# Performance work log

Hardware: AMD Instinct MI355X
Metric: run time of the kernel (lower is better)

Reference implementation:

```python
import jax, jax.numpy as jnp
import numpy as np

N, E = 50000, 800000
D_IN, H, D_OUT = 64, 64, 32
NEG_SLOPE = 0.2


def setup_inputs() -> dict:
    key = jax.random.key(0)
    ks = jax.random.split(key, 20)
    inp = {
        "x": jax.random.normal(ks[0], (N, D_IN), dtype=jnp.float32),
        "edge_index": jax.random.randint(ks[1], (2, E), 0, N, dtype=jnp.int32),
    }
    def lin(k, fan_in, fan_out):
        s = 1.0 / np.sqrt(fan_in)
        return jax.random.uniform(k, (fan_in, fan_out), jnp.float32, -s, s)
    # GAT layer params: W [in,H], att_src [H], att_dst [H], bias [H]
    dims_in = [D_IN, H, H]
    for i in range(3):
        inp[f"W{i+1}"] = lin(ks[2 + 4 * i], dims_in[i], H)
        inp[f"a_src{i+1}"] = jax.random.normal(ks[3 + 4 * i], (H,), jnp.float32) * 0.1
        inp[f"a_dst{i+1}"] = jax.random.normal(ks[4 + 4 * i], (H,), jnp.float32) * 0.1
        inp[f"b{i+1}"] = jnp.zeros((H,), jnp.float32)
    inp["lin1_W"] = lin(ks[14], H, H)
    inp["lin1_b"] = jnp.zeros((H,), jnp.float32)
    inp["lin2_W"] = lin(ks[15], H, D_OUT)
    inp["lin2_b"] = jnp.zeros((D_OUT,), jnp.float32)
    return inp


def gat_layer(x, src, dst, W, a_src, a_dst, b):
    h = x @ W                                   # [N, H]
    alpha_s = (h * a_src).sum(-1)               # [N]
    alpha_d = (h * a_dst).sum(-1)               # [N]
    e = jax.nn.leaky_relu(alpha_s[src] + alpha_d[dst], NEG_SLOPE)  # [E]
    m = jax.lax.stop_gradient(jax.ops.segment_max(e, dst, num_segments=N))
    w = jnp.exp(e - m[dst])                     # [E]
    denom = jax.ops.segment_sum(w, dst, num_segments=N)
    alpha = w / denom[dst]                      # segment softmax over incoming edges
    out = jax.ops.segment_sum(alpha[:, None] * h[src], dst, num_segments=N)
    return out + b


def reference(x, edge_index, W1, a_src1, a_dst1, b1, W2, a_src2, a_dst2, b2,
              W3, a_src3, a_dst3, b3, lin1_W, lin1_b, lin2_W, lin2_b):
    src, dst = edge_index[0], edge_index[1]
    h = jax.nn.relu(gat_layer(x, src, dst, W1, a_src1, a_dst1, b1))
    h = jax.nn.relu(gat_layer(h, src, dst, W2, a_src2, a_dst2, b2))
    h = jax.nn.relu(gat_layer(h, src, dst, W3, a_src3, a_dst3, b3))
    h = jax.nn.relu(h @ lin1_W + lin1_b)
    return h @ lin2_W + lin2_b
```

## Files before the change

kernel.cpp:

```cpp
#include <hip/hip_runtime.h>

#define NEG_SLOPE 0.2f
#define NBUCK 256

template <bool RELU, bool WANT_ALPHA>
__global__ __launch_bounds__(256) void gemm64(
    const float* __restrict__ x, const float* __restrict__ W,
    const float* __restrict__ bias,
    const float* __restrict__ a_src, const float* __restrict__ a_dst,
    float* __restrict__ out, float* __restrict__ alpha_s,
    float* __restrict__ alpha_d, int N)
{
    __shared__ float Xs[64][68];
    __shared__ float Ws[64][64];

    const int row0 = blockIdx.x * 64;

    for (int i = threadIdx.x; i < 1024; i += 256)
        ((float4*)Ws)[i] = ((const float4*)W)[i];
    for (int i = threadIdx.x; i < 1024; i += 256) {
        int r = i >> 4, c4 = (i & 15) * 4;
        float4 v = {0.f, 0.f, 0.f, 0.f};
        if (row0 + r < N) v = *(const float4*)&x[(size_t)(row0 + r) * 64 + c4];
        *(float4*)&Xs[r][c4] = v;
    }
    __syncthreads();

    const int tx = threadIdx.x & 15;
    const int ty = threadIdx.x >> 4;

    float acc[4][4] = {{0.f,0.f,0.f,0.f},{0.f,0.f,0.f,0.f},
                       {0.f,0.f,0.f,0.f},{0.f,0.f,0.f,0.f}};

#pragma unroll 8
    for (int k = 0; k < 64; ++k) {
        const float4 wv = *(const float4*)&Ws[k][tx * 4];
        const float x0 = Xs[ty * 4 + 0][k];
        const float x1 = Xs[ty * 4 + 1][k];
        const float x2 = Xs[ty * 4 + 2][k];
        const float x3 = Xs[ty * 4 + 3][k];
        acc[0][0] += x0 * wv.x; acc[0][1] += x0 * wv.y;
        acc[0][2] += x0 * wv.z; acc[0][3] += x0 * wv.w;
        acc[1][0] += x1 * wv.x; acc[1][1] += x1 * wv.y;
        acc[1][2] += x1 * wv.z; acc[1][3] += x1 * wv.w;
        acc[2][0] += x2 * wv.x; acc[2][1] += x2 * wv.y;
        acc[2][2] += x2 * wv.z; acc[2][3] += x2 * wv.w;
        acc[3][0] += x3 * wv.x; acc[3][1] += x3 * wv.y;
        acc[3][2] += x3 * wv.z; acc[3][3] += x3 * wv.w;
    }

    float4 bv = {0.f, 0.f, 0.f, 0.f};
    if (bias) bv = *(const float4*)&bias[tx * 4];

#pragma unroll
    for (int i = 0; i < 4; ++i) {
        const int r = row0 + ty * 4 + i;
        if (r < N) {
            float4 o;
            o.x = acc[i][0] + bv.x; o.y = acc[i][1] + bv.y;
            o.z = acc[i][2] + bv.z; o.w = acc[i][3] + bv.w;
            if (RELU) {
                o.x = fmaxf(o.x, 0.f); o.y = fmaxf(o.y, 0.f);
                o.z = fmaxf(o.z, 0.f); o.w = fmaxf(o.w, 0.f);
            }
            *(float4*)&out[(size_t)r * 64 + tx * 4] = o;
        }
    }

    if (WANT_ALPHA) {
        const float4 asv = *(const float4*)&a_src[tx * 4];
        const float4 adv = *(const float4*)&a_dst[tx * 4];
#pragma unroll
        for (int i = 0; i < 4; ++i) {
            float s = acc[i][0]*asv.x + acc[i][1]*asv.y
                    + acc[i][2]*asv.z + acc[i][3]*asv.w;
            float d = acc[i][0]*adv.x + acc[i][1]*adv.y
                    + acc[i][2]*adv.z + acc[i][3]*adv.w;
#pragma unroll
            for (int off = 1; off < 16; off <<= 1) {
                s += __shfl_xor(s, off, 16);
                d += __shfl_xor(d, off, 16);
            }
            const int r = row0 + ty * 4 + i;
            if (tx == 0 && r < N) { alpha_s[r] = s; alpha_d[r] = d; }
        }
    }
}

__global__ __launch_bounds__(256) void gemm_head(
    const float* __restrict__ X, const float* __restrict__ W1,
    const float* __restrict__ b1, const float* __restrict__ W2,
    const float* __restrict__ b2, float* __restrict__ out, int N)
{
    __shared__ float Xs[64][68];
    __shared__ float W1s[64][64];
    __shared__ float W2s[64][32];

    const int row0 = blockIdx.x * 64;

    for (int i = threadIdx.x; i < 1024; i += 256)
        ((float4*)W1s)[i] = ((const float4*)W1)[i];
    for (int i = threadIdx.x; i < 512; i += 256)
        ((float4*)W2s)[i] = ((const float4*)W2)[i];
    for (int i = threadIdx.x; i < 1024; i += 256) {
        int r = i >> 4, c4 = (i & 15) * 4;
        float4 v = {0.f, 0.f, 0.f, 0.f};
        if (row0 + r < N) v = *(const float4*)&X[(size_t)(row0 + r) * 64 + c4];
        *(float4*)&Xs[r][c4] = v;
    }
    __syncthreads();

    const int tx = threadIdx.x & 15;
    const int ty = threadIdx.x >> 4;

    float acc[4][4] = {{0,0,0,0},{0,0,0,0},{0,0,0,0},{0,0,0,0}};
#pragma unroll 8
    for (int k = 0; k < 64; ++k) {
        const float4 wv = *(const float4*)&W1s[k][tx * 4];
        const float x0 = Xs[ty * 4 + 0][k];
        const float x1 = Xs[ty * 4 + 1][k];
        const float x2 = Xs[ty * 4 + 2][k];
        const float x3 = Xs[ty * 4 + 3][k];
        acc[0][0] += x0 * wv.x; acc[0][1] += x0 * wv.y;
        acc[0][2] += x0 * wv.z; acc[0][3] += x0 * wv.w;
        acc[1][0] += x1 * wv.x; acc[1][1] += x1 * wv.y;
        acc[1][2] += x1 * wv.z; acc[1][3] += x1 * wv.w;
        acc[2][0] += x2 * wv.x; acc[2][1] += x2 * wv.y;
        acc[2][2] += x2 * wv.z; acc[2][3] += x2 * wv.w;
        acc[3][0] += x3 * wv.x; acc[3][1] += x3 * wv.y;
        acc[3][2] += x3 * wv.z; acc[3][3] += x3 * wv.w;
    }

    const float4 bv = *(const float4*)&b1[tx * 4];
    __syncthreads();
#pragma unroll
    for (int i = 0; i < 4; ++i) {
        Xs[ty * 4 + i][tx * 4 + 0] = fmaxf(acc[i][0] + bv.x, 0.f);
        Xs[ty * 4 + i][tx * 4 + 1] = fmaxf(acc[i][1] + bv.y, 0.f);
        Xs[ty * 4 + i][tx * 4 + 2] = fmaxf(acc[i][2] + bv.z, 0.f);
        Xs[ty * 4 + i][tx * 4 + 3] = fmaxf(acc[i][3] + bv.w, 0.f);
    }
    __syncthreads();

    float a2[4][2] = {{0,0},{0,0},{0,0},{0,0}};
#pragma unroll 8
    for (int k = 0; k < 64; ++k) {
        const float2 wv = *(const float2*)&W2s[k][tx * 2];
        const float t0 = Xs[ty * 4 + 0][k];
        const float t1 = Xs[ty * 4 + 1][k];
        const float t2 = Xs[ty * 4 + 2][k];
        const float t3 = Xs[ty * 4 + 3][k];
        a2[0][0] += t0 * wv.x; a2[0][1] += t0 * wv.y;
        a2[1][0] += t1 * wv.x; a2[1][1] += t1 * wv.y;
        a2[2][0] += t2 * wv.x; a2[2][1] += t2 * wv.y;
        a2[3][0] += t3 * wv.x; a2[3][1] += t3 * wv.y;
    }
    const float2 b2v = *(const float2*)&b2[tx * 2];
#pragma unroll
    for (int i = 0; i < 4; ++i) {
        const int r = row0 + ty * 4 + i;
        if (r < N) {
            float2 o;
            o.x = a2[i][0] + b2v.x;
            o.y = a2[i][1] + b2v.y;
            *(float2*)&out[(size_t)r * 32 + tx * 2] = o;
        }
    }
}

__global__ __launch_bounds__(256) void bucket_hist(
    const int* __restrict__ ei, int E, int* __restrict__ bhist)
{
    __shared__ int h[NBUCK];
    const int t = threadIdx.x;
    h[t] = 0;
    __syncthreads();
    for (int e = blockIdx.x * 256 + t; e < E; e += gridDim.x * 256)
        atomicAdd(&h[((unsigned)ei[E + e]) >> 8], 1);
    __syncthreads();
    if (h[t]) atomicAdd(&bhist[t], h[t]);
}

#define PC_EPT 8
#define PC_TILE 2048
__global__ __launch_bounds__(256) void partition_coarse(
    const int* __restrict__ ei, int E, const int* __restrict__ bhist,
    int* __restrict__ gcurs, int* __restrict__ pairs)
{
    __shared__ int sc[NBUCK];
    __shared__ int hist[NBUCK];
    __shared__ int base[NBUCK];
    const int t = threadIdx.x;

    const int bh = bhist[t];
    sc[t] = bh; __syncthreads();
    for (int off = 1; off < 256; off <<= 1) {
        int v = sc[t];
        if (t >= off) v += sc[t - off];
        __syncthreads(); sc[t] = v; __syncthreads();
    }
    const int bbase = sc[t] - bh;
    hist[t] = 0;
    __syncthreads();

    const int tile0 = blockIdx.x * PC_TILE;
    int sv[PC_EPT], dv[PC_EPT], rk[PC_EPT];
#pragma unroll
    for (int i = 0; i < PC_EPT; ++i) {
        const int e = tile0 + i * 256 + t;
        if (e < E) {
            sv[i] = ei[e];
            dv[i] = ei[E + e];
            rk[i] = atomicAdd(&hist[dv[i] >> 8], 1);
        } else dv[i] = -1;
    }
    __syncthreads();
    if (hist[t] > 0) base[t] = bbase + atomicAdd(&gcurs[t], hist[t]);
    __syncthreads();
#pragma unroll
    for (int i = 0; i < PC_EPT; ++i) {
        if (dv[i] >= 0) {
            const int b = dv[i] >> 8;
            pairs[base[b] + rk[i]] = sv[i] | ((dv[i] & 255) << 16);
        }
    }
}

__global__ __launch_bounds__(256) void fine_scatter(
    const int* __restrict__ bhist, const int* __restrict__ pairs,
    int N, int E, int* __restrict__ row_off, int* __restrict__ csr_src)
{
    __shared__ int sc[NBUCK];
    __shared__ int cnt[NBUCK];
    __shared__ int cur[NBUCK];
    const int t = threadIdx.x, b = blockIdx.x;

    const int bh = bhist[t];
    sc[t] = bh; __syncthreads();
    for (int off = 1; off < 256; off <<= 1) {
        int v = sc[t];
        if (t >= off) v += sc[t - off];
        __syncthreads(); sc[t] = v; __syncthreads();
    }
    sc[t] -= bh;
    cnt[t] = 0;
    __syncthreads();

    const int sb = sc[b];
    const int se = sb + bhist[b];

    for (int p = sb + t; p < se; p += 256)
        atomicAdd(&cnt[pairs[p] >> 16], 1);
    __syncthreads();

    const int c = cnt[t];
    cur[t] = c; __syncthreads();
    for (int off = 1; off < 256; off <<= 1) {
        int v = cur[t];
        if (t >= off) v += cur[t - off];
        __syncthreads(); cur[t] = v; __syncthreads();
    }
    const int node_off = sb + cur[t] - c;
    __syncthreads();
    cur[t] = node_off;
    const int n = b * 256 + t;
    if (n < N) row_off[n] = node_off;
    if (b == gridDim.x - 1 && t == 0) row_off[N] = E;
    __syncthreads();

    for (int p = sb + t; p < se; p += 256) {
        const int v = pairs[p];
        const int pos = atomicAdd(&cur[v >> 16], 1);
        csr_src[pos] = v & 0xFFFF;
    }
}

__global__ __launch_bounds__(256) void gat_aggregate(
    const int* __restrict__ row_off, const int* __restrict__ csr_src,
    const float* __restrict__ h, const float* __restrict__ as,
    const float* __restrict__ ad, const float* __restrict__ bias,
    float* __restrict__ out, int N)
{
    const int wv = (blockIdx.x * 256 + threadIdx.x) >> 6;
    if (wv >= N) return;
    const int d    = wv;
    const int lane = threadIdx.x & 63;
    const int g    = lane >> 4;
    const int gl   = lane & 15;

    const int beg = row_off[d], end = row_off[d + 1];
    const float add = ad[d];

    float  den  = 0.f;
    float4 acc0 = {0.f, 0.f, 0.f, 0.f};
    float4 acc1 = {0.f, 0.f, 0.f, 0.f};

    int s0 = (beg     + g < end) ? csr_src[beg     + g] : 0;
    int s1 = (beg + 4 + g < end) ? csr_src[beg + 4 + g] : 0;

    for (int e0 = beg; e0 < end; e0 += 8) {
        const bool v0 = (e0     + g < end);
        const bool v1 = (e0 + 4 + g < end);
        const int  cs0 = s0, cs1 = s1;

        const int n0 = e0 +  8 + g;
        const int n1 = e0 + 12 + g;
        s0 = (n0 < end) ? csr_src[n0] : 0;
        s1 = (n1 < end) ? csr_src[n1] : 0;

        const float4 h0 = *(const float4*)&h[(size_t)cs0 * 64 + gl * 4];
        const float4 h1 = *(const float4*)&h[(size_t)cs1 * 64 + gl * 4];
        const float  a0 = as[cs0];
        const float  a1 = as[cs1];

        float ev0 = a0 + add;
        ev0 = (ev0 >= 0.f) ? ev0 : NEG_SLOPE * ev0;
        float ev1 = a1 + add;
        ev1 = (ev1 >= 0.f) ? ev1 : NEG_SLOPE * ev1;

        const float w0 = v0 ? __expf(ev0) : 0.f;
        const float w1 = v1 ? __expf(ev1) : 0.f;

        den += w0 + w1;
        acc0.x += w0 * h0.x; acc0.y += w0 * h0.y;
        acc0.z += w0 * h0.z; acc0.w += w0 * h0.w;
        acc1.x += w1 * h1.x; acc1.y += w1 * h1.y;
        acc1.z += w1 * h1.z; acc1.w += w1 * h1.w;
    }

    float4 acc;
    acc.x = acc0.x + acc1.x; acc.y = acc0.y + acc1.y;
    acc.z = acc0.z + acc1.z; acc.w = acc0.w + acc1.w;

#pragma unroll
    for (int off = 16; off <= 32; off <<= 1) {
        acc.x += __shfl_xor(acc.x, off, 64);
        acc.y += __shfl_xor(acc.y, off, 64);
        acc.z += __shfl_xor(acc.z, off, 64);
        acc.w += __shfl_xor(acc.w, off, 64);
        den   += __shfl_xor(den,   off, 64);
    }

    if (g == 0) {
        const float4 bvv = *(const float4*)&bias[gl * 4];
        const float inv = (den > 0.f) ? (1.f / den) : 0.f;
        float4 o;
        o.x = fmaxf(acc.x * inv + bvv.x, 0.f);
        o.y = fmaxf(acc.y * inv + bvv.y, 0.f);
        o.z = fmaxf(acc.z * inv + bvv.z, 0.f);
        o.w = fmaxf(acc.w * inv + bvv.w, 0.f);
        *(float4*)&out[(size_t)d * 64 + gl * 4] = o;
    }
}

extern "C" void kernel_launch(void* const* d_in, const int* in_sizes, int n_in,
                              void* d_out, int out_size, void* d_ws, size_t ws_size,
                              hipStream_t stream)
{
    const float* x  = (const float*)d_in[0];
    const int*   ei = (const int*)d_in[1];
    const float* W[3]    = {(const float*)d_in[2], (const float*)d_in[6],  (const float*)d_in[10]};
    const float* asrc[3] = {(const float*)d_in[3], (const float*)d_in[7],  (const float*)d_in[11]};
    const float* adst[3] = {(const float*)d_in[4], (const float*)d_in[8],  (const float*)d_in[12]};
    const float* bia[3]  = {(const float*)d_in[5], (const float*)d_in[9],  (const float*)d_in[13]};
    const float* lin1W = (const float*)d_in[14];
    const float* lin1b = (const float*)d_in[15];
    const float* lin2W = (const float*)d_in[16];
    const float* lin2b = (const float*)d_in[17];

    const int N = in_sizes[0] / 64;
    const int E = in_sizes[1] / 2;
    const int B = (N + 255) / 256;

    float* X       = (float*)d_ws;
    float* H       = X + (size_t)N * 64;
    float* AS      = H + (size_t)N * 64;
    float* AD      = AS + N;
    int*   row_off = (int*)(AD + N);
    int*   csr_src = row_off + (N + 1);
    int*   bhist   = csr_src + E;
    int*   gcurs   = bhist + 256;
    int*   pairs   = (int*)H;

    const int g64_grid = (N + 63) / 64;
    const int agg_grid = (N + 3) / 4;
    const int pc_grid  = (E + PC_TILE - 1) / PC_TILE;

    hipMemsetAsync(bhist, 0, 512 * sizeof(int), stream);
    bucket_hist<<<256, 256, 0, stream>>>(ei, E, bhist);
    partition_coarse<<<pc_grid, 256, 0, stream>>>(ei, E, bhist, gcurs, pairs);
    fine_scatter<<<B, 256, 0, stream>>>(bhist, pairs, N, E, row_off, csr_src);

    for (int l = 0; l < 3; ++l) {
        const float* in_act = (l == 0) ? x : X;
        gemm64<false, true><<<g64_grid, 256, 0, stream>>>(
            in_act, W[l], nullptr, asrc[l], adst[l], H, AS, AD, N);
        gat_aggregate<<<agg_grid, 256, 0, stream>>>(
            row_off, csr_src, H, AS, AD, bia[l], X, N);
    }

    gemm_head<<<g64_grid, 256, 0, stream>>>(
        X, lin1W, lin1b, lin2W, lin2b, (float*)d_out, N);
}
```

Measured before the change: 209.2 us.

## Fuse bucket histogram into first GEMM and unroll aggregation to 16 edges

Removes the standalone bucket_hist kernel and folds the destination-bucket histogram into the first layer's gemm64 launch, run by its first 256 blocks. The pairs buffer moves out of H into its own workspace region so the layer-1 GEMM output survives partitioning. The aggregation loop now processes four edge groups per iteration instead of two, giving more independent gathers in flight per wave. Costs include an extra shared histogram buffer, extra registers in the aggregator, and a larger workspace.

```diff
diff --git a/kernel.cpp b/kernel.cpp
--- a/kernel.cpp
+++ b/kernel.cpp
@@ -3,16 +3,17 @@
 #define NEG_SLOPE 0.2f
 #define NBUCK 256
 
-template <bool RELU, bool WANT_ALPHA>
+template <bool WANT_ALPHA, bool DO_HIST>
 __global__ __launch_bounds__(256) void gemm64(
     const float* __restrict__ x, const float* __restrict__ W,
-    const float* __restrict__ bias,
     const float* __restrict__ a_src, const float* __restrict__ a_dst,
     float* __restrict__ out, float* __restrict__ alpha_s,
-    float* __restrict__ alpha_d, int N)
+    float* __restrict__ alpha_d, int N,
+    const int* __restrict__ ei, int E, int* __restrict__ bhist)
 {
     __shared__ float Xs[64][68];
     __shared__ float Ws[64][64];
+    __shared__ int   hsh[NBUCK];
 
     const int row0 = blockIdx.x * 64;
 
@@ -24,6 +25,7 @@
         if (row0 + r < N) v = *(const float4*)&x[(size_t)(row0 + r) * 64 + c4];
         *(float4*)&Xs[r][c4] = v;
     }
+    if (DO_HIST && blockIdx.x < 256) hsh[threadIdx.x] = 0;
     __syncthreads();
 
     const int tx = threadIdx.x & 15;
@@ -49,20 +51,11 @@
         acc[3][2] += x3 * wv.z; acc[3][3] += x3 * wv.w;
     }
 
-    float4 bv = {0.f, 0.f, 0.f, 0.f};
-    if (bias) bv = *(const float4*)&bias[tx * 4];
-
 #pragma unroll
     for (int i = 0; i < 4; ++i) {
         const int r = row0 + ty * 4 + i;
         if (r < N) {
-            float4 o;
-            o.x = acc[i][0] + bv.x; o.y = acc[i][1] + bv.y;
-            o.z = acc[i][2] + bv.z; o.w = acc[i][3] + bv.w;
-            if (RELU) {
-                o.x = fmaxf(o.x, 0.f); o.y = fmaxf(o.y, 0.f);
-                o.z = fmaxf(o.z, 0.f); o.w = fmaxf(o.w, 0.f);
-            }
+            float4 o = {acc[i][0], acc[i][1], acc[i][2], acc[i][3]};
             *(float4*)&out[(size_t)r * 64 + tx * 4] = o;
         }
     }
@@ -84,6 +77,14 @@
             const int r = row0 + ty * 4 + i;
             if (tx == 0 && r < N) { alpha_s[r] = s; alpha_d[r] = d; }
         }
+    }
+
+    if (DO_HIST && blockIdx.x < 256) {
+        __syncthreads();
+        for (int e = blockIdx.x * 256 + threadIdx.x; e < E; e += 256 * 256)
+            atomicAdd(&hsh[((unsigned)ei[E + e]) >> 8], 1);
+        __syncthreads();
+        if (hsh[threadIdx.x]) atomicAdd(&bhist[threadIdx.x], hsh[threadIdx.x]);
     }
 }
 
@@ -168,19 +169,6 @@
     }
 }
 
-__global__ __launch_bounds__(256) void bucket_hist(
-    const int* __restrict__ ei, int E, int* __restrict__ bhist)
-{
-    __shared__ int h[NBUCK];
-    const int t = threadIdx.x;
-    h[t] = 0;
-    __syncthreads();
-    for (int e = blockIdx.x * 256 + t; e < E; e += gridDim.x * 256)
-        atomicAdd(&h[((unsigned)ei[E + e]) >> 8], 1);
-    __syncthreads();
-    if (h[t]) atomicAdd(&bhist[t], h[t]);
-}
-
 #define PC_EPT 8
 #define PC_TILE 2048
 __global__ __launch_bounds__(256) void partition_coarse(
@@ -292,45 +280,61 @@
     const float add = ad[d];
 
     float  den  = 0.f;
-    float4 acc0 = {0.f, 0.f, 0.f, 0.f};
-    float4 acc1 = {0.f, 0.f, 0.f, 0.f};
-
-    int s0 = (beg     + g < end) ? csr_src[beg     + g] : 0;
-    int s1 = (beg + 4 + g < end) ? csr_src[beg + 4 + g] : 0;
-
-    for (int e0 = beg; e0 < end; e0 += 8) {
-        const bool v0 = (e0     + g < end);
-        const bool v1 = (e0 + 4 + g < end);
-        const int  cs0 = s0, cs1 = s1;
-
-        const int n0 = e0 +  8 + g;
-        const int n1 = e0 + 12 + g;
-        s0 = (n0 < end) ? csr_src[n0] : 0;
-        s1 = (n1 < end) ? csr_src[n1] : 0;
+    float4 acc0 = {0.f,0.f,0.f,0.f}, acc1 = {0.f,0.f,0.f,0.f};
+    float4 acc2 = {0.f,0.f,0.f,0.f}, acc3 = {0.f,0.f,0.f,0.f};
+
+    int s0 = (beg      + g < end) ? csr_src[beg      + g] : 0;
+    int s1 = (beg +  4 + g < end) ? csr_src[beg +  4 + g] : 0;
+    int s2 = (beg +  8 + g < end) ? csr_src[beg +  8 + g] : 0;
+    int s3 = (beg + 12 + g < end) ? csr_src[beg + 12 + g] : 0;
+
+    for (int e0 = beg; e0 < end; e0 += 16) {
+        const bool v0 = (e0      + g < end);
+        const bool v1 = (e0 +  4 + g < end);
+        const bool v2 = (e0 +  8 + g < end);
+        const bool v3 = (e0 + 12 + g < end);
+        const int cs0 = s0, cs1 = s1, cs2 = s2, cs3 = s3;
+
+        s0 = (e0 + 16 + g < end) ? csr_src[e0 + 16 + g] : 0;
+        s1 = (e0 + 20 + g < end) ? csr_src[e0 + 20 + g] : 0;
+        s2 = (e0 + 24 + g < end) ? csr_src[e0 + 24 + g] : 0;
+        s3 = (e0 + 28 + g < end) ? csr_src[e0 + 28 + g] : 0;
 
         const float4 h0 = *(const float4*)&h[(size_t)cs0 * 64 + gl * 4];
         const float4 h1 = *(const float4*)&h[(size_t)cs1 * 64 + gl * 4];
+        const float4 h2 = *(const float4*)&h[(size_t)cs2 * 64 + gl * 4];
+        const float4 h3 = *(const float4*)&h[(size_t)cs3 * 64 + gl * 4];
         const float  a0 = as[cs0];
         const float  a1 = as[cs1];
-
-        float ev0 = a0 + add;
-        ev0 = (ev0 >= 0.f) ? ev0 : NEG_SLOPE * ev0;
-        float ev1 = a1 + add;
-        ev1 = (ev1 >= 0.f) ? ev1 : NEG_SLOPE * ev1;
-
-        const float w0 = v0 ? __expf(ev0) : 0.f;
-        const float w1 = v1 ? __expf(ev1) : 0.f;
-
-        den += w0 + w1;
+        const float  a2 = as[cs2];
+        const float  a3 = as[cs3];
+
+        float e0v = a0 + add; e0v = (e0v >= 0.f) ? e0v : NEG_SLOPE * e0v;
+        float e1v = a1 + add; e1v = (e1v >= 0.f) ? e1v : NEG_SLOPE * e1v;
+        float e2v = a2 + add; e2v = (e2v >= 0.f) ? e2v : NEG_SLOPE * e2v;
+        float e3v = a3 + add; e3v = (e3v >= 0.f) ? e3v : NEG_SLOPE * e3v;
+
+        const float w0 = v0 ? __expf(e0v) : 0.f;
+        const float w1 = v1 ? __expf(e1v) : 0.f;
+        const float w2 = v2 ? __expf(e2v) : 0.f;
+        const float w3 = v3 ? __expf(e3v) : 0.f;
+
+        den += (w0 + w1) + (w2 + w3);
         acc0.x += w0 * h0.x; acc0.y += w0 * h0.y;
         acc0.z += w0 * h0.z; acc0.w += w0 * h0.w;
         acc1.x += w1 * h1.x; acc1.y += w1 * h1.y;
         acc1.z += w1 * h1.z; acc1.w += w1 * h1.w;
+        acc2.x += w2 * h2.x; acc2.y += w2 * h2.y;
+        acc2.z += w2 * h2.z; acc2.w += w2 * h2.w;
+        acc3.x += w3 * h3.x; acc3.y += w3 * h3.y;
+        acc3.z += w3 * h3.z; acc3.w += w3 * h3.w;
     }
 
     float4 acc;
-    acc.x = acc0.x + acc1.x; acc.y = acc0.y + acc1.y;
-    acc.z = acc0.z + acc1.z; acc.w = acc0.w + acc1.w;
+    acc.x = (acc0.x + acc1.x) + (acc2.x + acc3.x);
+    acc.y = (acc0.y + acc1.y) + (acc2.y + acc3.y);
+    acc.z = (acc0.z + acc1.z) + (acc2.z + acc3.z);
+    acc.w = (acc0.w + acc1.w) + (acc2.w + acc3.w);
 
 #pragma unroll
     for (int off = 16; off <= 32; off <<= 1) {
@@ -380,21 +384,26 @@
     int*   csr_src = row_off + (N + 1);
     int*   bhist   = csr_src + E;
     int*   gcurs   = bhist + 256;
-    int*   pairs   = (int*)H;
+    int*   pairs   = gcurs + 256;
 
     const int g64_grid = (N + 63) / 64;
     const int agg_grid = (N + 3) / 4;
     const int pc_grid  = (E + PC_TILE - 1) / PC_TILE;
 
     hipMemsetAsync(bhist, 0, 512 * sizeof(int), stream);
-    bucket_hist<<<256, 256, 0, stream>>>(ei, E, bhist);
+
+    gemm64<true, true><<<g64_grid, 256, 0, stream>>>(
+        x, W[0], asrc[0], adst[0], H, AS, AD, N, ei, E, bhist);
+
     partition_coarse<<<pc_grid, 256, 0, stream>>>(ei, E, bhist, gcurs, pairs);
     fine_scatter<<<B, 256, 0, stream>>>(bhist, pairs, N, E, row_off, csr_src);
 
-    for (int l = 0; l < 3; ++l) {
-        const float* in_act = (l == 0) ? x : X;
-        gemm64<false, true><<<g64_grid, 256, 0, stream>>>(
-            in_act, W[l], nullptr, asrc[l], adst[l], H, AS, AD, N);
+    gat_aggregate<<<agg_grid, 256, 0, stream>>>(
+        row_off, csr_src, H, AS, AD, bia[0], X, N);
+
+    for (int l = 1; l < 3; ++l) {
+        gemm64<true, false><<<g64_grid, 256, 0, stream>>>(
+            X, W[l], asrc[l], adst[l], H, AS, AD, N, nullptr, 0, nullptr);
         gat_aggregate<<<agg_grid, 256, 0, stream>>>(
             row_off, csr_src, H, AS, AD, bia[l], X, N);
     }
```

Result: faster. 202.6 us, median of 2 (-3.1%).
